# Performance work log

Hardware: AMD Instinct MI355X
Metric: run time of the kernel (lower is better)

The kernel has to match this reference:

```python
import jax, jax.numpy as jnp
import numpy as np

N = 50000      # nodes
E = 800000     # edges (before self-loops)
D = 128        # input_dim
H = 128        # hidden_dim
G = 256        # graphs in batch


def setup_inputs() -> dict:
    key = jax.random.key(0)
    ks = jax.random.split(key, 6)
    x = jax.random.normal(ks[0], (N, D), dtype=jnp.float32)
    edge_index = jax.random.randint(ks[1], (2, E), 0, N, dtype=jnp.int32)
    batch = jnp.sort(jax.random.randint(ks[2], (N,), 0, G, dtype=jnp.int32))
    W1 = jax.random.normal(ks[3], (D, H), dtype=jnp.float32) / np.sqrt(D).astype(np.float32)
    b1 = jnp.zeros((H,), jnp.float32)
    W2 = jax.random.normal(ks[4], (H, H), dtype=jnp.float32) / np.sqrt(H).astype(np.float32)
    b2 = jnp.zeros((H,), jnp.float32)
    alpha = jnp.full((H,), 0.25, jnp.float32)  # PReLU(hidden_dim) init
    return dict(x=x, edge_index=edge_index, batch=batch,
                W1=W1, b1=b1, W2=W2, b2=b2, alpha=alpha)


def _gcn_layer(z, W, b, src, dst, norm):
    # GCNConv: z' = D^{-1/2}(A+I)D^{-1/2} (z W) + b
    zw = z @ W                                            # [N,H] dense GEMM
    agg = jnp.zeros_like(zw).at[dst].add(norm[:, None] * zw[src])  # scatter-add over edges
    return agg + b


def reference(x, edge_index, batch, W1, b1, W2, b2, alpha):
    loop = jnp.arange(N, dtype=edge_index.dtype)
    src = jnp.concatenate([edge_index[0], loop])          # add self-loops
    dst = jnp.concatenate([edge_index[1], loop])
    deg = jnp.zeros((N,), x.dtype).at[dst].add(jnp.float32(1.0))
    dinv = jnp.where(deg > 0, jax.lax.rsqrt(deg), 0.0)
    norm = dinv[src] * dinv[dst]                          # [E+N] edge weights

    zs = []
    z = x
    for (W, b) in ((W1, b1), (W2, b2)):
        z = _gcn_layer(z, W, b, src, dst, norm)
        z = jnp.where(z > 0, z, alpha * z)                # channel-wise PReLU (shared)
        zs.append(z)

    gs = [jax.ops.segment_sum(zi, batch, num_segments=G) for zi in zs]  # global_add_pool
    g = jnp.concatenate(gs, axis=1)                       # [G, num_layers*H]
    return z, g
```

## Files before the change

kernel.cpp:

```cpp
#include <hip/hip_runtime.h>
#include <stdint.h>


#define CAP 96

typedef __attribute__((ext_vector_type(8))) short short8;
typedef __attribute__((ext_vector_type(4))) float f32x4;

__device__ __forceinline__ uint16_t bf16rne(float f) {
    uint32_t u = __float_as_uint(f);
    uint32_t r = (u + 0x7fffu + ((u >> 16) & 1u)) >> 16;
    return (uint16_t)r;
}
__device__ __forceinline__ float bf_lo(uint32_t v) { return __uint_as_float(v << 16); }
__device__ __forceinline__ float bf_hi(uint32_t v) { return __uint_as_float(v & 0xffff0000u); }

__global__ __launch_bounds__(512) void k0(int* __restrict__ cursor, int nbC, int N,
                                          const float* __restrict__ W1,
                                          const float* __restrict__ W2,
                                          uint16_t* __restrict__ Wf1,
                                          uint16_t* __restrict__ Wf2,
                                          float* __restrict__ g_out, int nbZ,
                                          uint32_t* __restrict__ zw) {
    int bid = blockIdx.x, t = threadIdx.x;
    if (bid < nbC) {
        int i = bid * 512 + t;
        if (i <= N) cursor[i] = 0;
        if (bid == 0 && t < 64) zw[(size_t)N * 64 + t] = 0u;
    } else if (bid < nbC + 8) {
        int tid = (bid - nbC) * 512 + t;
        const float* W = (tid & 2048) ? W2 : W1;
        uint16_t* O = (tid & 2048) ? Wf2 : Wf1;
        int q16 = tid & 2047;
        int lane = q16 & 63, n0ks = q16 >> 6;
        int n0 = n0ks >> 2, ks = n0ks & 3;
        int m = lane & 15, quad = lane >> 4;
        int nn = n0 * 16 + m;
        int kkb = ks * 32 + quad * 8;
        uint16_t v[8];
#pragma unroll
        for (int j = 0; j < 8; ++j) v[j] = bf16rne(W[(kkb + j) * 128 + nn]);
        *(short8*)&O[q16 * 8] = *(short8*)v;
    } else {
        int idx = (bid - nbC - 8) * 512 + t;
        ((float4*)g_out)[idx] = make_float4(0.f, 0.f, 0.f, 0.f);
    }
}

__device__ __forceinline__ void gemm_body(const float* Xf, const uint16_t* Xb,
                                          const uint16_t* __restrict__ Wf,
                                          uint16_t* __restrict__ Y, int nrows,
                                          const int* __restrict__ cnt,
                                          uint16_t* Wl, int bid, int t) {
    int lane = t & 63, w = t >> 6;
    int row0 = bid * 128;
    for (int c = t; c < 2048; c += 512)
        *(short8*)&Wl[c * 8] = *(const short8*)&Wf[c * 8];
    int m = lane & 15, quad = lane >> 4;
    int arow = row0 + w * 16 + m;
    bool rowok = arow < nrows;
    short8 a[4];
    short8 zer = {0, 0, 0, 0, 0, 0, 0, 0};
    if (Xb) {
        const uint16_t* aptr = Xb + (size_t)arow * 128 + quad * 8;
#pragma unroll
        for (int ks = 0; ks < 4; ++ks)
            a[ks] = rowok ? *(const short8*)(aptr + ks * 32) : zer;
    } else {
        const float* ap = Xf + (size_t)arow * 128 + quad * 8;
#pragma unroll
        for (int ks = 0; ks < 4; ++ks) {
            if (rowok) {
                float4 u0 = *(const float4*)(ap + ks * 32);
                float4 u1 = *(const float4*)(ap + ks * 32 + 4);
                uint32_t q[4];
                q[0] = (uint32_t)bf16rne(u0.x) | ((uint32_t)bf16rne(u0.y) << 16);
                q[1] = (uint32_t)bf16rne(u0.z) | ((uint32_t)bf16rne(u0.w) << 16);
                q[2] = (uint32_t)bf16rne(u1.x) | ((uint32_t)bf16rne(u1.y) << 16);
                q[3] = (uint32_t)bf16rne(u1.z) | ((uint32_t)bf16rne(u1.w) << 16);
                a[ks] = *(short8*)q;
            } else a[ks] = zer;
        }
    }
    __syncthreads();

    f32x4 acc[8];
#pragma unroll
    for (int i = 0; i < 8; ++i) acc[i] = (f32x4){0.f, 0.f, 0.f, 0.f};
#pragma unroll
    for (int ks = 0; ks < 4; ++ks)
#pragma unroll
        for (int n0 = 0; n0 < 8; ++n0) {
            short8 b = *(short8*)&Wl[((n0 * 4 + ks) * 64 + lane) * 8];
            acc[n0] = __builtin_amdgcn_mfma_f32_16x16x32_bf16(a[ks], b, acc[n0], 0, 0, 0);
        }
    __syncthreads();

    float dsc[4] = {1.f, 1.f, 1.f, 1.f};
    if (cnt) {
#pragma unroll
        for (int r = 0; r < 4; ++r) {
            int gr = row0 + w * 16 + quad * 4 + r;
            int d = (gr < nrows) ? cnt[gr] : 0;
            dsc[r] = rsqrtf((float)(d + 1));
        }
    }

    uint16_t* Ep = Wl;
#pragma unroll
    for (int n0 = 0; n0 < 8; ++n0)
#pragma unroll
        for (int r = 0; r < 4; ++r)
            Ep[(w * 16 + quad * 4 + r) * 136 + n0 * 16 + m] = bf16rne(acc[n0][r] * dsc[r]);
    for (int r16 = 0; r16 < 16; ++r16) {
        int row = row0 + w * 16 + r16;
        if (row < nrows) {
            uint32_t v = *(uint32_t*)&Ep[(w * 16 + r16) * 136 + lane * 2];
            ((uint32_t*)Y)[(size_t)row * 64 + lane] = v;
        }
    }
}

__device__ __forceinline__ void fill_body(const int* __restrict__ src, const int* __restrict__ dst,
                                          int* __restrict__ cursor, uint16_t* __restrict__ col,
                                          int E, int fb, int t) {
    int base = fb * 2048 + t;
    int d[4], s[4], p[4];
#pragma unroll
    for (int k = 0; k < 4; ++k) {
        int e = base + k * 512;
        d[k] = (e < E) ? dst[e] : -1;
        s[k] = (e < E) ? src[e] : 0;
    }
#pragma unroll
    for (int k = 0; k < 4; ++k) if (d[k] >= 0) p[k] = atomicAdd(&cursor[d[k]], 1);
#pragma unroll
    for (int k = 0; k < 4; ++k)
        if (d[k] >= 0 && p[k] < CAP) col[(size_t)d[k] * CAP + p[k]] = (uint16_t)s[k];
}

__global__ __launch_bounds__(512, 8) void k5(const float* __restrict__ X,
                                             const uint16_t* __restrict__ Wf,
                                             uint16_t* __restrict__ Y, int nrows, int gemmGrid,
                                             const int* __restrict__ src, const int* __restrict__ dst,
                                             int* __restrict__ cursor, uint16_t* __restrict__ col,
                                             int E, int fillGrid) {
    __shared__ uint16_t Wl[17408];
    int bid = blockIdx.x, t = threadIdx.x;
    int mn = min(gemmGrid, fillGrid), mn2 = 2 * mn;
    int role, idx;
    if (bid < mn2) { role = bid & 1; idx = bid >> 1; }
    else { role = (gemmGrid > fillGrid) ? 0 : 1; idx = bid - mn2 + mn; }
    if (role == 0) gemm_body(X, nullptr, Wf, Y, nrows, nullptr, Wl, idx, t);
    else fill_body(src, dst, cursor, col, E, idx, t);
}

__global__ __launch_bounds__(512, 8) void gemm2k(const uint16_t* __restrict__ Xb,
                                                 const uint16_t* __restrict__ Wf,
                                                 uint16_t* __restrict__ Y, int nrows,
                                                 const int* __restrict__ cnt) {
    __shared__ uint16_t Wl[17408];
    gemm_body(nullptr, Xb, Wf, Y, nrows, cnt, Wl, blockIdx.x, threadIdx.x);
}

__global__ __launch_bounds__(512) void zscale(uint32_t* __restrict__ zw,
                                              const int* __restrict__ cnt, int ndw) {
    int idx = blockIdx.x * 512 + threadIdx.x;
    if (idx >= ndw) return;
    int row = idx >> 6;
    float di = rsqrtf((float)(cnt[row] + 1));
    uint32_t v = zw[idx];
    float lo = bf_lo(v) * di, hi = bf_hi(v) * di;
    zw[idx] = (uint32_t)bf16rne(lo) | ((uint32_t)bf16rne(hi) << 16);
}

template <bool PS>
__global__ __launch_bounds__(256) void aggp(const uint32_t* __restrict__ zw,
                                            const int* __restrict__ cnt,
                                            const uint16_t* __restrict__ col,
                                            const float* __restrict__ bias,
                                            const float* __restrict__ alpha,
                                            const int* __restrict__ batch,
                                            float* __restrict__ gout, int col_off,
                                            uint32_t* __restrict__ z1b,
                                            float* __restrict__ zoutf,
                                            int mode, int n) {
    __shared__ int gsh[4];
    __shared__ float red[4][128];
    int wv = threadIdx.x >> 6;
    int lane = threadIdx.x & 63;
    int node = blockIdx.x * 4 + wv;
    bool valid = node < n;
    int nc = __builtin_amdgcn_readfirstlane(valid ? node : (n - 1));
    int c = lane * 2;
    int deg = cnt[nc];
    float di = rsqrtf((float)(deg + 1));
    uint32_t sv = zw[(size_t)nc * 64 + lane];
    float sw = PS ? 1.f : di;
    float ax = sw * bf_lo(sv), ay = sw * bf_hi(sv);
    float bx = 0.f, by = 0.f;
    int len = min(deg, CAP);
    int len8 = (len + 7) & ~7;
    const uint32_t* cbu = (const uint32_t*)(col + (size_t)nc * CAP);
    uint32_t cc = cbu[lane < 48 ? lane : 0];
    for (int e = 0; e < len8; e += 8) {
        int h = e >> 1;
        uint32_t q0 = (uint32_t)__builtin_amdgcn_readlane((int)cc, h);
        uint32_t q1 = (uint32_t)__builtin_amdgcn_readlane((int)cc, h + 1);
        uint32_t q2 = (uint32_t)__builtin_amdgcn_readlane((int)cc, h + 2);
        uint32_t q3 = (uint32_t)__builtin_amdgcn_readlane((int)cc, h + 3);
        int s0 = (e + 0 < len) ? (int)(q0 & 0xffffu) : n;
        int s1 = (e + 1 < len) ? (int)(q0 >> 16)     : n;
        int s2 = (e + 2 < len) ? (int)(q1 & 0xffffu) : n;
        int s3 = (e + 3 < len) ? (int)(q1 >> 16)     : n;
        int s4 = (e + 4 < len) ? (int)(q2 & 0xffffu) : n;
        int s5 = (e + 5 < len) ? (int)(q2 >> 16)     : n;
        int s6 = (e + 6 < len) ? (int)(q3 & 0xffffu) : n;
        int s7 = (e + 7 < len) ? (int)(q3 >> 16)     : n;
        uint32_t v0 = zw[(size_t)s0 * 64 + lane];
        uint32_t v1 = zw[(size_t)s1 * 64 + lane];
        uint32_t v2 = zw[(size_t)s2 * 64 + lane];
        uint32_t v3 = zw[(size_t)s3 * 64 + lane];
        uint32_t v4 = zw[(size_t)s4 * 64 + lane];
        uint32_t v5 = zw[(size_t)s5 * 64 + lane];
        uint32_t v6 = zw[(size_t)s6 * 64 + lane];
        uint32_t v7 = zw[(size_t)s7 * 64 + lane];
        float w0 = PS ? 1.f : rsqrtf((float)(cnt[s0] + 1));
        float w1 = PS ? 1.f : rsqrtf((float)(cnt[s1] + 1));
        float w2 = PS ? 1.f : rsqrtf((float)(cnt[s2] + 1));
        float w3 = PS ? 1.f : rsqrtf((float)(cnt[s3] + 1));
        float w4 = PS ? 1.f : rsqrtf((float)(cnt[s4] + 1));
        float w5 = PS ? 1.f : rsqrtf((float)(cnt[s5] + 1));
        float w6 = PS ? 1.f : rsqrtf((float)(cnt[s6] + 1));
        float w7 = PS ? 1.f : rsqrtf((float)(cnt[s7] + 1));
        ax += w0 * bf_lo(v0); ay += w0 * bf_hi(v0);
        bx += w1 * bf_lo(v1); by += w1 * bf_hi(v1);
        ax += w2 * bf_lo(v2); ay += w2 * bf_hi(v2);
        bx += w3 * bf_lo(v3); by += w3 * bf_hi(v3);
        ax += w4 * bf_lo(v4); ay += w4 * bf_hi(v4);
        bx += w5 * bf_lo(v5); by += w5 * bf_hi(v5);
        ax += w6 * bf_lo(v6); ay += w6 * bf_hi(v6);
        bx += w7 * bf_lo(v7); by += w7 * bf_hi(v7);
    }
    ax += bx; ay += by;
    float zx = di * ax + bias[c];
    float zy = di * ay + bias[c + 1];
    float px = alpha[c], py = alpha[c + 1];
    zx = zx > 0.f ? zx : px * zx;
    zy = zy > 0.f ? zy : py * zy;

    if (valid) {
        if (mode == 0) {
            uint32_t pk = (uint32_t)bf16rne(zx) | ((uint32_t)bf16rne(zy) << 16);
            z1b[(size_t)nc * 64 + lane] = pk;
        } else {
            ((float2*)zoutf)[(size_t)nc * 64 + lane] = make_float2(zx, zy);
        }
    }

    int g = batch[nc];
    float cx = valid ? zx : 0.f, cy = valid ? zy : 0.f;
    if (lane == 0) gsh[wv] = valid ? g : -1 - wv;
    __syncthreads();
    bool uni = (gsh[0] == gsh[1]) && (gsh[1] == gsh[2]) && (gsh[2] == gsh[3]);
    if (uni) {
        red[wv][c] = cx; red[wv][c + 1] = cy;
        __syncthreads();
        if (wv == 0) {
            float sx = red[0][c] + red[1][c] + red[2][c] + red[3][c];
            float sy = red[0][c + 1] + red[1][c + 1] + red[2][c + 1] + red[3][c + 1];
            float* base = &gout[(size_t)g * 256 + col_off];
            atomicAdd(&base[c], sx);
            atomicAdd(&base[c + 1], sy);
        }
    } else {
        __syncthreads();
        if (valid) {
            float* base = &gout[(size_t)g * 256 + col_off];
            atomicAdd(&base[c], cx);
            atomicAdd(&base[c + 1], cy);
        }
    }
}

extern "C" void kernel_launch(void* const* d_in, const int* in_sizes, int n_in,
                              void* d_out, int out_size, void* d_ws, size_t ws_size,
                              hipStream_t stream) {
    const float* x     = (const float*)d_in[0];
    const int*   eidx  = (const int*)d_in[1];
    const int*   batch = (const int*)d_in[2];
    const float* W1    = (const float*)d_in[3];
    const float* b1    = (const float*)d_in[4];
    const float* W2    = (const float*)d_in[5];
    const float* b2    = (const float*)d_in[6];
    const float* alpha = (const float*)d_in[7];

    const int N = in_sizes[2];
    const int E = in_sizes[1] / 2;
    const int G = (out_size - N * 128) / 256;

    const int* src = eidx;
    const int* dst = eidx + E;

    char* ws = (char*)d_ws;
    size_t off = 0;
    auto alloc = [&](size_t bytes) { void* q = ws + off; off = (off + bytes + 255) & ~(size_t)255; return q; };
    int*      cursor = (int*)alloc((size_t)(N + 1) * 4);
    uint16_t* col    = (uint16_t*)alloc((size_t)N * CAP * 2);
    uint32_t* zw     = (uint32_t*)alloc((size_t)(N + 1) * 128 * 2);
    uint32_t* z1b    = (uint32_t*)alloc((size_t)N * 128 * 2);
    uint16_t* Wf1    = (uint16_t*)alloc(128 * 128 * 2);
    uint16_t* Wf2    = (uint16_t*)alloc(128 * 128 * 2);

    float* z_out = (float*)d_out;
    float* g_out = (float*)d_out + (size_t)N * 128;

    int nbC      = (N + 512) / 512;
    int nbZ      = (G * 256 / 4 + 511) / 512;
    int fillGrid = (E + 2047) / 2048;
    int gemmGrid = (N + 127) / 128;
    int aggGrid  = (N + 3) / 4;
    int ndw      = N * 64;
    int zsGrid   = (ndw + 511) / 512;

    k0<<<nbC + 8 + nbZ, 512, 0, stream>>>(cursor, nbC, N, W1, W2, Wf1, Wf2, g_out, nbZ, zw);
    k5<<<gemmGrid + fillGrid, 512, 0, stream>>>(x, Wf1, (uint16_t*)zw, N, gemmGrid,
                                                src, dst, cursor, col, E, fillGrid);
    zscale<<<zsGrid, 512, 0, stream>>>(zw, cursor, ndw);
    aggp<true><<<aggGrid, 256, 0, stream>>>(zw, cursor, col, b1, alpha, batch,
                                            g_out, 0, z1b, nullptr, 0, N);
    gemm2k<<<gemmGrid, 512, 0, stream>>>((const uint16_t*)z1b, Wf2, (uint16_t*)zw, N, cursor);
    aggp<true><<<aggGrid, 256, 0, stream>>>(zw, cursor, col, b2, alpha, batch,
                                            g_out, 128, nullptr, z_out, 1, N);
}
```

Measured before the change: 226.8 us.

## Process four nodes per wave in aggregation and halve edges per fill block

The aggregation kernel now has each wave handle four consecutive nodes instead of one. It prefetches the degrees, self rows and neighbor lists for all four up front, then accumulates the per-graph pooling sum in registers. The block-wide graph uniformity check now uses the batch ids of the first and last node, so one shared-memory reduction and one set of atomics covers 16 nodes rather than 4. Separately, the fill phase in the fused GEMM/fill kernel now handles 2 edges per thread instead of 4, doubling the fill grid to spread the atomics across more blocks. The costs are fewer aggregation blocks with more serial work per wave, and a fallback to per-node atomics whenever a block spans a graph boundary.

```diff
diff --git a/kernel.cpp b/kernel.cpp
--- a/kernel.cpp
+++ b/kernel.cpp
@@ -124,18 +124,18 @@
 __device__ __forceinline__ void fill_body(const int* __restrict__ src, const int* __restrict__ dst,
                                           int* __restrict__ cursor, uint16_t* __restrict__ col,
                                           int E, int fb, int t) {
-    int base = fb * 2048 + t;
-    int d[4], s[4], p[4];
-#pragma unroll
-    for (int k = 0; k < 4; ++k) {
+    int base = fb * 1024 + t;
+    int d[2], s[2], p[2];
+#pragma unroll
+    for (int k = 0; k < 2; ++k) {
         int e = base + k * 512;
         d[k] = (e < E) ? dst[e] : -1;
         s[k] = (e < E) ? src[e] : 0;
     }
 #pragma unroll
-    for (int k = 0; k < 4; ++k) if (d[k] >= 0) p[k] = atomicAdd(&cursor[d[k]], 1);
-#pragma unroll
-    for (int k = 0; k < 4; ++k)
+    for (int k = 0; k < 2; ++k) if (d[k] >= 0) p[k] = atomicAdd(&cursor[d[k]], 1);
+#pragma unroll
+    for (int k = 0; k < 2; ++k)
         if (d[k] >= 0 && p[k] < CAP) col[(size_t)d[k] * CAP + p[k]] = (uint16_t)s[k];
 }
 
@@ -185,100 +185,113 @@
                                             uint32_t* __restrict__ z1b,
                                             float* __restrict__ zoutf,
                                             int mode, int n) {
-    __shared__ int gsh[4];
     __shared__ float red[4][128];
     int wv = threadIdx.x >> 6;
     int lane = threadIdx.x & 63;
-    int node = blockIdx.x * 4 + wv;
-    bool valid = node < n;
-    int nc = __builtin_amdgcn_readfirstlane(valid ? node : (n - 1));
     int c = lane * 2;
-    int deg = cnt[nc];
-    float di = rsqrtf((float)(deg + 1));
-    uint32_t sv = zw[(size_t)nc * 64 + lane];
-    float sw = PS ? 1.f : di;
-    float ax = sw * bf_lo(sv), ay = sw * bf_hi(sv);
-    float bx = 0.f, by = 0.f;
-    int len = min(deg, CAP);
-    int len8 = (len + 7) & ~7;
-    const uint32_t* cbu = (const uint32_t*)(col + (size_t)nc * CAP);
-    uint32_t cc = cbu[lane < 48 ? lane : 0];
-    for (int e = 0; e < len8; e += 8) {
-        int h = e >> 1;
-        uint32_t q0 = (uint32_t)__builtin_amdgcn_readlane((int)cc, h);
-        uint32_t q1 = (uint32_t)__builtin_amdgcn_readlane((int)cc, h + 1);
-        uint32_t q2 = (uint32_t)__builtin_amdgcn_readlane((int)cc, h + 2);
-        uint32_t q3 = (uint32_t)__builtin_amdgcn_readlane((int)cc, h + 3);
-        int s0 = (e + 0 < len) ? (int)(q0 & 0xffffu) : n;
-        int s1 = (e + 1 < len) ? (int)(q0 >> 16)     : n;
-        int s2 = (e + 2 < len) ? (int)(q1 & 0xffffu) : n;
-        int s3 = (e + 3 < len) ? (int)(q1 >> 16)     : n;
-        int s4 = (e + 4 < len) ? (int)(q2 & 0xffffu) : n;
-        int s5 = (e + 5 < len) ? (int)(q2 >> 16)     : n;
-        int s6 = (e + 6 < len) ? (int)(q3 & 0xffffu) : n;
-        int s7 = (e + 7 < len) ? (int)(q3 >> 16)     : n;
-        uint32_t v0 = zw[(size_t)s0 * 64 + lane];
-        uint32_t v1 = zw[(size_t)s1 * 64 + lane];
-        uint32_t v2 = zw[(size_t)s2 * 64 + lane];
-        uint32_t v3 = zw[(size_t)s3 * 64 + lane];
-        uint32_t v4 = zw[(size_t)s4 * 64 + lane];
-        uint32_t v5 = zw[(size_t)s5 * 64 + lane];
-        uint32_t v6 = zw[(size_t)s6 * 64 + lane];
-        uint32_t v7 = zw[(size_t)s7 * 64 + lane];
-        float w0 = PS ? 1.f : rsqrtf((float)(cnt[s0] + 1));
-        float w1 = PS ? 1.f : rsqrtf((float)(cnt[s1] + 1));
-        float w2 = PS ? 1.f : rsqrtf((float)(cnt[s2] + 1));
-        float w3 = PS ? 1.f : rsqrtf((float)(cnt[s3] + 1));
-        float w4 = PS ? 1.f : rsqrtf((float)(cnt[s4] + 1));
-        float w5 = PS ? 1.f : rsqrtf((float)(cnt[s5] + 1));
-        float w6 = PS ? 1.f : rsqrtf((float)(cnt[s6] + 1));
-        float w7 = PS ? 1.f : rsqrtf((float)(cnt[s7] + 1));
-        ax += w0 * bf_lo(v0); ay += w0 * bf_hi(v0);
-        bx += w1 * bf_lo(v1); by += w1 * bf_hi(v1);
-        ax += w2 * bf_lo(v2); ay += w2 * bf_hi(v2);
-        bx += w3 * bf_lo(v3); by += w3 * bf_hi(v3);
-        ax += w4 * bf_lo(v4); ay += w4 * bf_hi(v4);
-        bx += w5 * bf_lo(v5); by += w5 * bf_hi(v5);
-        ax += w6 * bf_lo(v6); ay += w6 * bf_hi(v6);
-        bx += w7 * bf_lo(v7); by += w7 * bf_hi(v7);
-    }
-    ax += bx; ay += by;
-    float zx = di * ax + bias[c];
-    float zy = di * ay + bias[c + 1];
-    float px = alpha[c], py = alpha[c + 1];
-    zx = zx > 0.f ? zx : px * zx;
-    zy = zy > 0.f ? zy : py * zy;
-
-    if (valid) {
-        if (mode == 0) {
-            uint32_t pk = (uint32_t)bf16rne(zx) | ((uint32_t)bf16rne(zy) << 16);
-            z1b[(size_t)nc * 64 + lane] = pk;
-        } else {
-            ((float2*)zoutf)[(size_t)nc * 64 + lane] = make_float2(zx, zy);
-        }
-    }
-
-    int g = batch[nc];
-    float cx = valid ? zx : 0.f, cy = valid ? zy : 0.f;
-    if (lane == 0) gsh[wv] = valid ? g : -1 - wv;
-    __syncthreads();
-    bool uni = (gsh[0] == gsh[1]) && (gsh[1] == gsh[2]) && (gsh[2] == gsh[3]);
+    int b0 = blockIdx.x * 16;
+    int base = b0 + wv * 4;
+    int g0 = batch[min(b0, n - 1)];
+    int gL = batch[min(b0 + 15, n - 1)];
+    bool uni = (g0 == gL);
+    float bsx = bias[c], bsy = bias[c + 1];
+    float pax = alpha[c], pay = alpha[c + 1];
+
+    int nd[4], dg[4];
+    uint32_t sv[4], cc[4];
+#pragma unroll
+    for (int q = 0; q < 4; ++q) {
+        int node = base + q;
+        nd[q] = (node < n) ? node : n;
+        dg[q] = cnt[nd[q]];
+        sv[q] = zw[(size_t)nd[q] * 64 + lane];
+        cc[q] = ((const uint32_t*)(col + (size_t)nd[q] * CAP))[lane < 48 ? lane : 0];
+    }
+
+    float psx = 0.f, psy = 0.f;
+#pragma unroll
+    for (int q = 0; q < 4; ++q) {
+        int node = base + q;
+        bool valid = node < n;
+        float di = rsqrtf((float)(dg[q] + 1));
+        float sw = PS ? 1.f : di;
+        float ax = sw * bf_lo(sv[q]), ay = sw * bf_hi(sv[q]);
+        float bx = 0.f, by = 0.f;
+        int len = min(dg[q], CAP);
+        int len8 = (len + 7) & ~7;
+        for (int e = 0; e < len8; e += 8) {
+            int h = e >> 1;
+            uint32_t q0 = (uint32_t)__builtin_amdgcn_readlane((int)cc[q], h);
+            uint32_t q1 = (uint32_t)__builtin_amdgcn_readlane((int)cc[q], h + 1);
+            uint32_t q2 = (uint32_t)__builtin_amdgcn_readlane((int)cc[q], h + 2);
+            uint32_t q3 = (uint32_t)__builtin_amdgcn_readlane((int)cc[q], h + 3);
+            int s0 = (e + 0 < len) ? (int)(q0 & 0xffffu) : n;
+            int s1 = (e + 1 < len) ? (int)(q0 >> 16)     : n;
+            int s2 = (e + 2 < len) ? (int)(q1 & 0xffffu) : n;
+            int s3 = (e + 3 < len) ? (int)(q1 >> 16)     : n;
+            int s4 = (e + 4 < len) ? (int)(q2 & 0xffffu) : n;
+            int s5 = (e + 5 < len) ? (int)(q2 >> 16)     : n;
+            int s6 = (e + 6 < len) ? (int)(q3 & 0xffffu) : n;
+            int s7 = (e + 7 < len) ? (int)(q3 >> 16)     : n;
+            uint32_t v0 = zw[(size_t)s0 * 64 + lane];
+            uint32_t v1 = zw[(size_t)s1 * 64 + lane];
+            uint32_t v2 = zw[(size_t)s2 * 64 + lane];
+            uint32_t v3 = zw[(size_t)s3 * 64 + lane];
+            uint32_t v4 = zw[(size_t)s4 * 64 + lane];
+            uint32_t v5 = zw[(size_t)s5 * 64 + lane];
+            uint32_t v6 = zw[(size_t)s6 * 64 + lane];
+            uint32_t v7 = zw[(size_t)s7 * 64 + lane];
+            float w0 = PS ? 1.f : rsqrtf((float)(cnt[s0] + 1));
+            float w1 = PS ? 1.f : rsqrtf((float)(cnt[s1] + 1));
+            float w2 = PS ? 1.f : rsqrtf((float)(cnt[s2] + 1));
+            float w3 = PS ? 1.f : rsqrtf((float)(cnt[s3] + 1));
+            float w4 = PS ? 1.f : rsqrtf((float)(cnt[s4] + 1));
+            float w5 = PS ? 1.f : rsqrtf((float)(cnt[s5] + 1));
+            float w6 = PS ? 1.f : rsqrtf((float)(cnt[s6] + 1));
+            float w7 = PS ? 1.f : rsqrtf((float)(cnt[s7] + 1));
+            ax += w0 * bf_lo(v0); ay += w0 * bf_hi(v0);
+            bx += w1 * bf_lo(v1); by += w1 * bf_hi(v1);
+            ax += w2 * bf_lo(v2); ay += w2 * bf_hi(v2);
+            bx += w3 * bf_lo(v3); by += w3 * bf_hi(v3);
+            ax += w4 * bf_lo(v4); ay += w4 * bf_hi(v4);
+            bx += w5 * bf_lo(v5); by += w5 * bf_hi(v5);
+            ax += w6 * bf_lo(v6); ay += w6 * bf_hi(v6);
+            bx += w7 * bf_lo(v7); by += w7 * bf_hi(v7);
+        }
+        ax += bx; ay += by;
+        float zx = di * ax + bsx;
+        float zy = di * ay + bsy;
+        zx = zx > 0.f ? zx : pax * zx;
+        zy = zy > 0.f ? zy : pay * zy;
+
+        if (valid) {
+            if (mode == 0) {
+                uint32_t pk = (uint32_t)bf16rne(zx) | ((uint32_t)bf16rne(zy) << 16);
+                z1b[(size_t)node * 64 + lane] = pk;
+            } else {
+                ((float2*)zoutf)[(size_t)node * 64 + lane] = make_float2(zx, zy);
+            }
+        }
+        float cx = valid ? zx : 0.f, cy = valid ? zy : 0.f;
+        if (uni) {
+            psx += cx; psy += cy;
+        } else if (valid) {
+            int gr = batch[node];
+            float* bp = &gout[(size_t)gr * 256 + col_off];
+            atomicAdd(&bp[c], cx);
+            atomicAdd(&bp[c + 1], cy);
+        }
+    }
+
     if (uni) {
-        red[wv][c] = cx; red[wv][c + 1] = cy;
+        red[wv][c] = psx; red[wv][c + 1] = psy;
         __syncthreads();
         if (wv == 0) {
             float sx = red[0][c] + red[1][c] + red[2][c] + red[3][c];
             float sy = red[0][c + 1] + red[1][c + 1] + red[2][c + 1] + red[3][c + 1];
-            float* base = &gout[(size_t)g * 256 + col_off];
-            atomicAdd(&base[c], sx);
-            atomicAdd(&base[c + 1], sy);
-        }
-    } else {
-        __syncthreads();
-        if (valid) {
-            float* base = &gout[(size_t)g * 256 + col_off];
-            atomicAdd(&base[c], cx);
-            atomicAdd(&base[c + 1], cy);
+            float* bp = &gout[(size_t)g0 * 256 + col_off];
+            atomicAdd(&bp[c], sx);
+            atomicAdd(&bp[c + 1], sy);
         }
     }
 }
@@ -317,9 +330,9 @@
 
     int nbC      = (N + 512) / 512;
     int nbZ      = (G * 256 / 4 + 511) / 512;
-    int fillGrid = (E + 2047) / 2048;
+    int fillGrid = (E + 1023) / 1024;
     int gemmGrid = (N + 127) / 128;
-    int aggGrid  = (N + 3) / 4;
+    int aggGrid  = (N + 15) / 16;
     int ndw      = N * 64;
     int zsGrid   = (ndw + 511) / 512;
 
```

After: 210.9 us. 7.0% less time.
